# Optimization experiments

Measured on AMD Instinct MI355X. Metric: run time of the kernel, lower is better.

Reference implementation:

```python
import jax, jax.numpy as jnp
import numpy as np

MARGINS = jnp.array([0.1, 0.085, 0.07, 0.04], dtype=jnp.float32)
EPS = 1e-6  # torch F.pairwise_distance adds eps to the difference


def setup_inputs() -> dict:
    key = jax.random.key(0)
    k1, k2, k3, k4 = jax.random.split(key, 4)
    B, D = 262144, 128
    return {
        "anchors": jax.random.normal(k1, (B, D), dtype=jnp.float32),
        "poss": jax.random.normal(k2, (B, D), dtype=jnp.float32),
        "negs": jax.random.normal(k3, (B, D), dtype=jnp.float32),
        "cs": jax.random.randint(k4, (B,), 0, 4, dtype=jnp.int64),
    }


def reference(anchors, poss, negs, cs):
    # d(x, y) = || x - y + eps ||_2  (matches torch pairwise_distance, p=2)
    d_ap = jnp.sqrt(jnp.sum(jnp.square(anchors - poss + EPS), axis=-1))  # [B]
    d_an = jnp.sqrt(jnp.sum(jnp.square(anchors - negs + EPS), axis=-1))  # [B]
    margins = MARGINS[cs]  # per-sample margin, [B]
    loss = jnp.maximum(d_ap - d_an + margins, 0.0)
    return jnp.mean(loss)
```

## Files before the change

### kernel.cpp

```cpp
#include <hip/hip_runtime.h>


#define TL_D 128
#define TL_BLOCK 256
#define TL_GRID 2048

__device__ __forceinline__ float tl_margin(int c) {
    return (c == 0) ? 0.10f
         : (c == 1) ? 0.085f
         : (c == 2) ? 0.07f
         : 0.04f;
}

#define TL_ACC(av, bv, dst)                           \
    {                                                 \
        float _d;                                     \
        _d = (av).x - (bv).x + 1e-6f; dst += _d * _d; \
        _d = (av).y - (bv).y + 1e-6f; dst += _d * _d; \
        _d = (av).z - (bv).z + 1e-6f; dst += _d * _d; \
        _d = (av).w - (bv).w + 1e-6f; dst += _d * _d; \
    }

__global__ __launch_bounds__(TL_BLOCK) void triplet_partial_kernel(
    const float* __restrict__ a,
    const float* __restrict__ p,
    const float* __restrict__ n,
    const int* __restrict__ cs32,
    float* __restrict__ partials,
    int nrows)
{
    const int tid    = threadIdx.x;
    const int lane32 = tid & 31;
    const int G      = blockIdx.x * (TL_BLOCK / 32) + (tid >> 5);
    const int TG     = gridDim.x * (TL_BLOCK / 32);

    float local = 0.0f;

    int row = G;
    float4 aC, pC, nC;
    int cC = 0;
    if (row < nrows) {
        const size_t base = (size_t)row * TL_D + lane32 * 4;
        aC = *reinterpret_cast<const float4*>(a + base);
        pC = *reinterpret_cast<const float4*>(p + base);
        nC = *reinterpret_cast<const float4*>(n + base);
        cC = cs32[2 * (size_t)row];
    }

    while (row < nrows) {
        const int nrow = row + TG;
        const int lrow = (nrow < nrows) ? nrow : row;
        const size_t nb = (size_t)lrow * TL_D + lane32 * 4;
        const float4 aN = *reinterpret_cast<const float4*>(a + nb);
        const float4 pN = *reinterpret_cast<const float4*>(p + nb);
        const float4 nN = *reinterpret_cast<const float4*>(n + nb);
        const int    cN = cs32[2 * (size_t)lrow];

        float dap = 0.0f, dan = 0.0f;
        TL_ACC(aC, pC, dap);
        TL_ACC(aC, nC, dan);

        #pragma unroll
        for (int m = 1; m <= 16; m <<= 1) {
            dap += __shfl_xor(dap, m, 64);
            dan += __shfl_xor(dan, m, 64);
        }

        if (lane32 == 0) {
            local += fmaxf(sqrtf(dap) - sqrtf(dan) + tl_margin(cC), 0.0f);
        }

        row = nrow;
        aC = aN; pC = pN; nC = nN; cC = cN;
    }

    local += __shfl_xor(local, 32, 64);

    __shared__ float swave[TL_BLOCK / 64];
    if ((tid & 63) == 0) swave[tid >> 6] = local;
    __syncthreads();
    if (tid == 0) {
        float s = 0.0f;
        #pragma unroll
        for (int w = 0; w < TL_BLOCK / 64; ++w) s += swave[w];
        partials[blockIdx.x] = s;
    }
}

__global__ __launch_bounds__(TL_BLOCK) void triplet_final_kernel(
    const float* __restrict__ partials,
    int nparts,
    float* __restrict__ out,
    float invB)
{
    __shared__ float sdata[TL_BLOCK];
    float local = 0.0f;
    for (int i = threadIdx.x; i < nparts; i += TL_BLOCK) local += partials[i];
    sdata[threadIdx.x] = local;
    __syncthreads();
    #pragma unroll
    for (int s = TL_BLOCK / 2; s > 0; s >>= 1) {
        if (threadIdx.x < s) sdata[threadIdx.x] += sdata[threadIdx.x + s];
        __syncthreads();
    }
    if (threadIdx.x == 0) out[0] = sdata[0] * invB;
}

extern "C" void kernel_launch(void* const* d_in, const int* in_sizes, int n_in,
                              void* d_out, int out_size, void* d_ws, size_t ws_size,
                              hipStream_t stream)
{
    const float* a    = (const float*)d_in[0];
    const float* p    = (const float*)d_in[1];
    const float* n    = (const float*)d_in[2];
    const int*   cs32 = (const int*)d_in[3];
    float*       out  = (float*)d_out;
    float*       partials = (float*)d_ws;

    const int nrows = in_sizes[3];

    int nblocks = TL_GRID;
    const int maxParts = (int)(ws_size / sizeof(float));
    if (nblocks > maxParts) nblocks = maxParts;
    if (nblocks < 1) nblocks = 1;

    triplet_partial_kernel<<<nblocks, TL_BLOCK, 0, stream>>>(a, p, n, cs32, partials, nrows);
    triplet_final_kernel<<<1, TL_BLOCK, 0, stream>>>(partials, nblocks, out, 1.0f / (float)nrows);
}
```

Baseline: 76.52 us.

## Fuse final reduction into main kernel via last-block atomic counter and halve shuffles

Replaces the separate final-reduction kernel with a last-block-done pattern: each block writes its partial, increments an atomic counter, and the last block reduces all partials and writes the mean. The per-row reduction also packs the ap and an sums into one value per lane pair, so the butterfly needs roughly half as many shuffles. A hipMemsetAsync resets the counter before every launch, which adds a stream operation in exchange for removing one kernel launch.

```diff
diff --git a/kernel.cpp b/kernel.cpp
--- a/kernel.cpp
+++ b/kernel.cpp
@@ -21,13 +21,15 @@
         _d = (av).w - (bv).w + 1e-6f; dst += _d * _d; \
     }
 
-__global__ __launch_bounds__(TL_BLOCK) void triplet_partial_kernel(
+__global__ __launch_bounds__(TL_BLOCK) void triplet_fused_kernel(
     const float* __restrict__ a,
     const float* __restrict__ p,
     const float* __restrict__ n,
     const int* __restrict__ cs32,
     float* __restrict__ partials,
-    int nrows)
+    unsigned int* __restrict__ counter,
+    float* __restrict__ out,
+    int nrows, float invB)
 {
     const int tid    = threadIdx.x;
     const int lane32 = tid & 31;
@@ -60,14 +62,15 @@
         TL_ACC(aC, pC, dap);
         TL_ACC(aC, nC, dan);
 
+        const float od = __shfl_xor(dap, 1, 64);
+        const float on = __shfl_xor(dan, 1, 64);
+        float v = (lane32 & 1) ? (dan + on) : (dap + od);
         #pragma unroll
-        for (int m = 1; m <= 16; m <<= 1) {
-            dap += __shfl_xor(dap, m, 64);
-            dan += __shfl_xor(dan, m, 64);
-        }
-
+        for (int m = 2; m <= 16; m <<= 1) v += __shfl_xor(v, m, 64);
+        const float sq = sqrtf(v);
+        const float other = __shfl_xor(sq, 1, 64);
         if (lane32 == 0) {
-            local += fmaxf(sqrtf(dap) - sqrtf(dan) + tl_margin(cC), 0.0f);
+            local += fmaxf(sq - other + tl_margin(cC), 0.0f);
         }
 
         row = nrow;
@@ -77,6 +80,7 @@
     local += __shfl_xor(local, 32, 64);
 
     __shared__ float swave[TL_BLOCK / 64];
+    __shared__ int sIsLast;
     if ((tid & 63) == 0) swave[tid >> 6] = local;
     __syncthreads();
     if (tid == 0) {
@@ -84,26 +88,28 @@
         #pragma unroll
         for (int w = 0; w < TL_BLOCK / 64; ++w) s += swave[w];
         partials[blockIdx.x] = s;
+        __threadfence();
+        const unsigned int prev =
+            __hip_atomic_fetch_add(counter, 1u, __ATOMIC_ACQ_REL,
+                                   __HIP_MEMORY_SCOPE_AGENT);
+        sIsLast = (prev == gridDim.x - 1) ? 1 : 0;
     }
-}
+    __syncthreads();
 
-__global__ __launch_bounds__(TL_BLOCK) void triplet_final_kernel(
-    const float* __restrict__ partials,
-    int nparts,
-    float* __restrict__ out,
-    float invB)
-{
-    __shared__ float sdata[TL_BLOCK];
-    float local = 0.0f;
-    for (int i = threadIdx.x; i < nparts; i += TL_BLOCK) local += partials[i];
-    sdata[threadIdx.x] = local;
-    __syncthreads();
-    #pragma unroll
-    for (int s = TL_BLOCK / 2; s > 0; s >>= 1) {
-        if (threadIdx.x < s) sdata[threadIdx.x] += sdata[threadIdx.x + s];
+    if (sIsLast) {
+        __threadfence();
+        float s = 0.0f;
+        for (int i = tid; i < (int)gridDim.x; i += TL_BLOCK) s += partials[i];
+        __shared__ float sdata[TL_BLOCK];
+        sdata[tid] = s;
         __syncthreads();
+        #pragma unroll
+        for (int st = TL_BLOCK / 2; st > 0; st >>= 1) {
+            if (tid < st) sdata[tid] += sdata[tid + st];
+            __syncthreads();
+        }
+        if (tid == 0) out[0] = sdata[0] * invB;
     }
-    if (threadIdx.x == 0) out[0] = sdata[0] * invB;
 }
 
 extern "C" void kernel_launch(void* const* d_in, const int* in_sizes, int n_in,
@@ -115,15 +121,19 @@
     const float* n    = (const float*)d_in[2];
     const int*   cs32 = (const int*)d_in[3];
     float*       out  = (float*)d_out;
-    float*       partials = (float*)d_ws;
 
     const int nrows = in_sizes[3];
 
+    float* partials = (float*)d_ws;
+    unsigned int* counter = (unsigned int*)((char*)d_ws + TL_GRID * sizeof(float));
+
     int nblocks = TL_GRID;
-    const int maxParts = (int)(ws_size / sizeof(float));
+    const int maxParts = (int)((ws_size - sizeof(unsigned int)) / sizeof(float));
     if (nblocks > maxParts) nblocks = maxParts;
     if (nblocks < 1) nblocks = 1;
 
-    triplet_partial_kernel<<<nblocks, TL_BLOCK, 0, stream>>>(a, p, n, cs32, partials, nrows);
-    triplet_final_kernel<<<1, TL_BLOCK, 0, stream>>>(partials, nblocks, out, 1.0f / (float)nrows);
+    hipMemsetAsync((void*)counter, 0, sizeof(unsigned int), stream);
+
+    triplet_fused_kernel<<<nblocks, TL_BLOCK, 0, stream>>>(
+        a, p, n, cs32, partials, counter, out, nrows, 1.0f / (float)nrows);
 }
```

Measured after the change: 260.4 us. +240.3%, slower.
